# Kernel tuning notes

Measured on AMD Instinct MI355X. Metric: run time of the kernel, lower is better.

## Reference

```python
import jax, jax.numpy as jnp
import numpy as np

B, S, H, NH, I = 8, 1024, 1024, 16, 4096
HD = H // NH
EPS = 1e-6
NEG = -1e9


def _glorot(key, shape):
    lim = np.sqrt(6.0 / (shape[0] + shape[1]))
    return jax.random.uniform(key, shape, jnp.float32, -lim, lim)


def setup_inputs() -> dict:
    key = jax.random.key(0)
    ks = jax.random.split(key, 8)
    return {
        "inputs": jax.random.normal(ks[0], (B, S, H), jnp.float32),
        "inputs_mask": jnp.zeros((B, S), jnp.float32),  # 1.0 marks padding
        "attn_qkvw": _glorot(ks[1], (H, 3 * H)),
        "attn_qkvb": jnp.zeros((3 * H,), jnp.float32),
        "attn_ow": _glorot(ks[2], (H, H)),
        "attn_ob": jnp.zeros((H,), jnp.float32),
        "attn_nw": jnp.ones((H,), jnp.float32),
        "attn_nb": jnp.zeros((H,), jnp.float32),
        "inter_w": _glorot(ks[3], (H, I)),
        "inter_b": jnp.zeros((I,), jnp.float32),
        "output_w": _glorot(ks[4], (I, H)),
        "output_b": jnp.zeros((H,), jnp.float32),
        "ffn_nw": jnp.ones((H,), jnp.float32),
        "ffn_nb": jnp.zeros((H,), jnp.float32),
    }


def _layer_norm(x, g, b):
    m = jnp.mean(x, axis=-1, keepdims=True)
    v = jnp.mean(jnp.square(x - m), axis=-1, keepdims=True)
    return (x - m) * jax.lax.rsqrt(v + EPS) * g + b


def reference(inputs, inputs_mask, attn_qkvw, attn_qkvb, attn_ow, attn_ob,
              attn_nw, attn_nb, inter_w, inter_b, output_w, output_b,
              ffn_nw, ffn_nb):
    # ---- self-attention block (pre-LN) ----
    res = inputs
    x = _layer_norm(inputs, attn_nw, attn_nb)
    qkv = x @ attn_qkvw + attn_qkvb                      # [B,S,3H]
    q, k, v = jnp.split(qkv, 3, axis=-1)
    q = q.reshape(B, S, NH, HD)
    k = k.reshape(B, S, NH, HD)
    v = v.reshape(B, S, NH, HD)
    scale = 1.0 / np.sqrt(HD)
    scores = jnp.einsum("bqhd,bkhd->bhqk", q, k) * scale
    scores = scores + inputs_mask[:, None, None, :] * NEG
    probs = jax.nn.softmax(scores, axis=-1)
    ctx = jnp.einsum("bhqk,bkhd->bqhd", probs, v).reshape(B, S, H)
    attn_out = ctx @ attn_ow + attn_ob
    x = res + attn_out
    # ---- FFN block (pre-LN, ReLU) ----
    res2 = x
    y = _layer_norm(x, ffn_nw, ffn_nb)
    h = jax.nn.relu(y @ inter_w + inter_b)
    return res2 + h @ output_w + output_b
```

## Files before the change

kernel.cpp:

```cpp
#include <hip/hip_runtime.h>
#include <cstdint>
#include <cstddef>

typedef _Float16 f16;
typedef _Float16 half8 __attribute__((ext_vector_type(8)));
typedef _Float16 half4v __attribute__((ext_vector_type(4)));
typedef float floatx4 __attribute__((ext_vector_type(4)));
typedef float floatx16 __attribute__((ext_vector_type(16)));

__device__ __forceinline__ floatx4 mfma16(half8 a, half8 b, floatx4 c) {
    return __builtin_amdgcn_mfma_f32_16x16x32_f16(a, b, c, 0, 0, 0);
}
__device__ __forceinline__ floatx16 mfma32(half8 a, half8 b, floatx16 c) {
    return __builtin_amdgcn_mfma_f32_32x32x16_f16(a, b, c, 0, 0, 0);
}

__device__ __forceinline__ void async16(const f16* g, f16* l) {
    __builtin_amdgcn_global_load_lds(
        (const __attribute__((address_space(1))) unsigned int*)(uintptr_t)g,
        (__attribute__((address_space(3))) unsigned int*)(uintptr_t)l,
        16, 0, 0);
}

__global__ __launch_bounds__(256)
void ln_f16_kernel(const float* __restrict__ x, const float* __restrict__ g,
                   const float* __restrict__ be, f16* __restrict__ y)
{
    int row = blockIdx.x, t = threadIdx.x;
    const float* xr = x + (size_t)row * 1024;
    float4 v = *(const float4*)(xr + t * 4);
    float s1 = v.x + v.y + v.z + v.w;
    float s2 = v.x * v.x + v.y * v.y + v.z * v.z + v.w * v.w;
    #pragma unroll
    for (int off = 32; off >= 1; off >>= 1) {
        s1 += __shfl_xor(s1, off);
        s2 += __shfl_xor(s2, off);
    }
    __shared__ float r1[4], r2[4];
    if ((t & 63) == 0) { r1[t >> 6] = s1; r2[t >> 6] = s2; }
    __syncthreads();
    s1 = r1[0] + r1[1] + r1[2] + r1[3];
    s2 = r2[0] + r2[1] + r2[2] + r2[3];
    float mean = s1 * 0.0009765625f;
    float var  = s2 * 0.0009765625f - mean * mean;
    float rs = rsqrtf(var + 1e-6f);
    float4 gv = *(const float4*)(g + t * 4);
    float4 bv = *(const float4*)(be + t * 4);
    half4v o;
    o[0] = (f16)((v.x - mean) * rs * gv.x + bv.x);
    o[1] = (f16)((v.y - mean) * rs * gv.y + bv.y);
    o[2] = (f16)((v.z - mean) * rs * gv.z + bv.z);
    o[3] = (f16)((v.w - mean) * rs * gv.w + bv.w);
    *(half4v*)(y + (size_t)row * 1024 + t * 4) = o;
}

__global__ __launch_bounds__(256)
void transpose_f16_kernel(const float* __restrict__ W, f16* __restrict__ WT,
                          int R, int C)
{
    __shared__ float tile[32][33];
    int tx = threadIdx.x & 31, ty0 = threadIdx.x >> 5;
    int r0 = blockIdx.y * 32, c0 = blockIdx.x * 32;
    #pragma unroll
    for (int i = 0; i < 4; ++i)
        tile[ty0 + i * 8][tx] = W[(size_t)(r0 + ty0 + i * 8) * C + c0 + tx];
    __syncthreads();
    #pragma unroll
    for (int i = 0; i < 4; ++i)
        WT[(size_t)(c0 + ty0 + i * 8) * R + r0 + tx] = (f16)tile[tx][ty0 + i * 8];
}

__global__ __launch_bounds__(256, 2)
void gemm_kernel(const f16* __restrict__ A, const f16* __restrict__ BT,
                 const float* __restrict__ bias, const float* __restrict__ res,
                 float* __restrict__ Cf32, int M, int N, int K)
{
    __shared__ __align__(16) f16 As[128 * 64];
    __shared__ __align__(16) f16 Bs[128 * 64];
    int m0 = blockIdx.x * 128, n0 = blockIdx.y * 128;
    int t = threadIdx.x, lane = t & 63, wave = t >> 6;
    int quad = lane >> 4, l16 = lane & 15;
    int wm = (wave & 1) * 64, wn = (wave >> 1) * 64;
    int sw = l16 & 7;
    floatx4 acc[4][4] = {};

    for (int k0 = 0; k0 < K; k0 += 64) {
        __syncthreads();
        #pragma unroll
        for (int c = 0; c < 4; ++c) {
            int s = c * 256 + t;
            int row = s >> 3, phys = s & 7;
            int lg = phys ^ (row & 7);
            async16(A  + (size_t)(m0 + row) * K + k0 + lg * 8,
                    As + (size_t)(c * 256 + (t & ~63)) * 8);
            async16(BT + (size_t)(n0 + row) * K + k0 + lg * 8,
                    Bs + (size_t)(c * 256 + (t & ~63)) * 8);
        }
        __syncthreads();
        #pragma unroll
        for (int ks = 0; ks < 2; ++ks) {
            int ca = (ks * 4 + quad) ^ sw;
            half8 a[4], b[4];
            #pragma unroll
            for (int i = 0; i < 4; ++i) {
                a[i] = *(const half8*)(As + (wm + i * 16 + l16) * 64 + ca * 8);
                b[i] = *(const half8*)(Bs + (wn + i * 16 + l16) * 64 + ca * 8);
            }
            #pragma unroll
            for (int i = 0; i < 4; ++i)
                #pragma unroll
                for (int j = 0; j < 4; ++j)
                    acc[i][j] = mfma16(a[i], b[j], acc[i][j]);
        }
    }

    #pragma unroll
    for (int j = 0; j < 4; ++j) {
        int col = n0 + wn + j * 16 + l16;
        float bv = bias[col];
        #pragma unroll
        for (int i = 0; i < 4; ++i) {
            int rowb = m0 + wm + i * 16 + quad * 4;
            #pragma unroll
            for (int r = 0; r < 4; ++r) {
                float v = acc[i][j][r] + bv;
                size_t idx = (size_t)(rowb + r) * N + col;
                Cf32[idx] = v + res[idx];
            }
        }
    }
}

template<int MODE>
__global__ __launch_bounds__(256, 2)
void gemm_big_kernel(const f16* __restrict__ A, const f16* __restrict__ BT,
                     const float* __restrict__ bias, f16* __restrict__ Cf16,
                     f16* __restrict__ qb, f16* __restrict__ kb, f16* __restrict__ vb,
                     int M, int N, int K)
{
    __shared__ __align__(16) f16 As[256 * 64];
    __shared__ __align__(16) f16 Bs[128 * 64];
    int m0 = blockIdx.x * 256, n0 = blockIdx.y * 128;
    int t = threadIdx.x, lane = t & 63, wave = t >> 6;
    int l32 = lane & 31, kg = lane >> 5;
    int swz = l32 & 7;
    floatx16 acc[2][4];
    #pragma unroll
    for (int mi = 0; mi < 2; ++mi)
        #pragma unroll
        for (int jn = 0; jn < 4; ++jn)
            #pragma unroll
            for (int r = 0; r < 16; ++r) acc[mi][jn][r] = 0.f;

    for (int k0 = 0; k0 < K; k0 += 64) {
        __syncthreads();
        #pragma unroll
        for (int c = 0; c < 8; ++c) {
            int s = c * 256 + t;
            int row = s >> 3, phys = s & 7;
            int lg = phys ^ (row & 7);
            async16(A + (size_t)(m0 + row) * K + k0 + lg * 8,
                    As + (size_t)(c * 256 + (t & ~63)) * 8);
        }
        #pragma unroll
        for (int c = 0; c < 4; ++c) {
            int s = c * 256 + t;
            int row = s >> 3, phys = s & 7;
            int lg = phys ^ (row & 7);
            async16(BT + (size_t)(n0 + row) * K + k0 + lg * 8,
                    Bs + (size_t)(c * 256 + (t & ~63)) * 8);
        }
        __syncthreads();
        #pragma unroll
        for (int ss = 0; ss < 4; ++ss) {
            int ca = (ss * 2 + kg) ^ swz;
            half8 a[2], b[4];
            #pragma unroll
            for (int mi = 0; mi < 2; ++mi)
                a[mi] = *(const half8*)(As + (wave * 64 + mi * 32 + l32) * 64 + ca * 8);
            #pragma unroll
            for (int jn = 0; jn < 4; ++jn)
                b[jn] = *(const half8*)(Bs + (jn * 32 + l32) * 64 + ca * 8);
            #pragma unroll
            for (int mi = 0; mi < 2; ++mi)
                #pragma unroll
                for (int jn = 0; jn < 4; ++jn)
                    acc[mi][jn] = mfma32(a[mi], b[jn], acc[mi][jn]);
        }
    }

    #pragma unroll
    for (int mi = 0; mi < 2; ++mi) {
        int mbase = m0 + wave * 64 + mi * 32 + 4 * kg;
        #pragma unroll
        for (int jn = 0; jn < 4; ++jn) {
            int col = n0 + jn * 32 + l32;
            float bv = bias[col];
            if (MODE == 1) {
                #pragma unroll
                for (int reg = 0; reg < 16; ++reg) {
                    int row = mbase + (reg & 3) + 8 * (reg >> 2);
                    Cf16[(size_t)row * N + col] = (f16)fmaxf(acc[mi][jn][reg] + bv, 0.f);
                }
            } else {
                int part = col >> 10;
                int h = (col >> 6) & 15;
                int d = col & 63;
                if (part == 2) {
                    #pragma unroll
                    for (int rb = 0; rb < 4; ++rb) {
                        int m = mbase + 8 * rb;
                        int bb = m >> 10, s = m & 1023;
                        size_t bh = (size_t)bb * 16 + h;
                        half4v pv;
                        #pragma unroll
                        for (int r = 0; r < 4; ++r) pv[r] = (f16)(acc[mi][jn][rb * 4 + r] + bv);
                        *(half4v*)(vb + (bh * 64 + d) * 1024 + s) = pv;
                    }
                } else {
                    f16* dst0 = part == 0 ? qb : kb;
                    #pragma unroll
                    for (int reg = 0; reg < 16; ++reg) {
                        int m = mbase + (reg & 3) + 8 * (reg >> 2);
                        int bb = m >> 10, s = m & 1023;
                        size_t bh = (size_t)bb * 16 + h;
                        dst0[(bh * 1024 + s) * 64 + d] = (f16)(acc[mi][jn][reg] + bv);
                    }
                }
            }
        }
    }
}

__global__ __launch_bounds__(256)
void attn_kernel(const f16* __restrict__ qb, const f16* __restrict__ kb,
                 const f16* __restrict__ vb, const float* __restrict__ mask,
                 f16* __restrict__ ctx)
{
    const int S = 1024;
    int qt = blockIdx.x, h = blockIdx.y, b = blockIdx.z;
    size_t bh = (size_t)b * 16 + h;
    int t = threadIdx.x, lane = t & 63, wv = t >> 6;
    int quad = lane >> 4, l16 = lane & 15;
    int sw = l16 & 7;

    __shared__ __align__(16) f16 Ks[64 * 64];
    __shared__ __align__(16) f16 Vs[64 * 64];
    __shared__ __align__(16) f16 Ps[4][16 * 40];

    int q0 = qt * 64 + wv * 16;
    const f16* qrow = qb + (bh * 1024 + q0 + l16) * 64;
    half8 aq0 = *(const half8*)(qrow + quad * 8);
    half8 aq1 = *(const half8*)(qrow + 32 + quad * 8);

    floatx4 o[4] = {};
    float lsum[4] = {0.f, 0.f, 0.f, 0.f};
    const float scale = 0.125f;
    const float* mrow = mask + b * S;

    for (int kc = 0; kc < S; kc += 64) {
        __syncthreads();
        #pragma unroll
        for (int c = 0; c < 2; ++c) {
            int s = c * 256 + t;
            int row = s >> 3, phys = s & 7;
            int lg = phys ^ (row & 7);
            f16* lk = Ks + (size_t)(c * 256 + (t & ~63)) * 8;
            f16* lv = Vs + (size_t)(c * 256 + (t & ~63)) * 8;
            async16(kb + (bh * 1024 + kc + row) * 64 + lg * 8, lk);
            async16(vb + (bh * 64 + row) * 1024 + kc + lg * 8, lv);
        }
        __syncthreads();

        floatx4 sf[4];
        #pragma unroll
        for (int cg = 0; cg < 4; ++cg) {
            const f16* kr = Ks + (cg * 16 + l16) * 64;
            int c0 = quad ^ sw;
            half8 b0 = *(const half8*)(kr + c0 * 8);
            half8 b1 = *(const half8*)(kr + (c0 ^ 4) * 8);
            floatx4 z = {};
            sf[cg] = mfma16(aq1, b1, mfma16(aq0, b0, z));
        }
        #pragma unroll
        for (int cg = 0; cg < 4; ++cg) {
            float mk = mrow[kc + cg * 16 + l16] * (-1e9f);
            #pragma unroll
            for (int r = 0; r < 4; ++r) {
                float e = __expf(sf[cg][r] * scale + mk);
                lsum[r] += e;
                Ps[wv][(quad * 4 + r) * 40 + cg * 16 + l16] = (f16)e;
            }
        }
        half8 ap0 = *(const half8*)(Ps[wv] + l16 * 40 + quad * 8);
        half8 ap1 = *(const half8*)(Ps[wv] + l16 * 40 + 32 + quad * 8);
        #pragma unroll
        for (int td = 0; td < 4; ++td) {
            const f16* vr = Vs + (td * 16 + l16) * 64;
            int c0 = quad ^ sw;
            half8 bv0 = *(const half8*)(vr + c0 * 8);
            half8 bv1 = *(const half8*)(vr + (c0 ^ 4) * 8);
            o[td] = mfma16(ap0, bv0, o[td]);
            o[td] = mfma16(ap1, bv1, o[td]);
        }
    }

    #pragma unroll
    for (int r = 0; r < 4; ++r) {
        float s = lsum[r];
        s += __shfl_xor(s, 1); s += __shfl_xor(s, 2);
        s += __shfl_xor(s, 4); s += __shfl_xor(s, 8);
        lsum[r] = 1.f / s;
    }
    #pragma unroll
    for (int td = 0; td < 4; ++td)
        #pragma unroll
        for (int r = 0; r < 4; ++r)
            ctx[((size_t)b * 1024 + q0 + quad * 4 + r) * 1024 + h * 64 + td * 16 + l16]
                = (f16)(o[td][r] * lsum[r]);
}

extern "C" void kernel_launch(void* const* d_in, const int* in_sizes, int n_in,
                              void* d_out, int out_size, void* d_ws, size_t ws_size,
                              hipStream_t stream)
{
    const float* inputs = (const float*)d_in[0];
    const float* mask   = (const float*)d_in[1];
    const float* qkvw   = (const float*)d_in[2];
    const float* qkvb   = (const float*)d_in[3];
    const float* ow     = (const float*)d_in[4];
    const float* ob     = (const float*)d_in[5];
    const float* anw    = (const float*)d_in[6];
    const float* anb    = (const float*)d_in[7];
    const float* iw     = (const float*)d_in[8];
    const float* ib     = (const float*)d_in[9];
    const float* outw   = (const float*)d_in[10];
    const float* outb   = (const float*)d_in[11];
    const float* fnw    = (const float*)d_in[12];
    const float* fnb    = (const float*)d_in[13];
    float* out = (float*)d_out;

    const int M = 8192;
    uint8_t* ws = (uint8_t*)d_ws;
    f16* wT_qkv = (f16*)(ws + 0);
    f16* wT_o   = (f16*)(ws + 6291456);
    f16* wT_i   = (f16*)(ws + 8388608);
    f16* wT_out = (f16*)(ws + 16777216);
    f16* xln    = (f16*)(ws + 25165824);
    float* x1   = (float*)(ws + 41943040);
    f16* qbuf   = (f16*)(ws + 75497472);
    f16* kbuf   = (f16*)(ws + 92274688);
    f16* vbuf   = (f16*)(ws + 109051904);
    f16* ctx    = (f16*)(ws + 125829120);
    f16* hbuf   = (f16*)(ws + 75497472);

    transpose_f16_kernel<<<dim3(96, 32),  256, 0, stream>>>(qkvw, wT_qkv, 1024, 3072);
    transpose_f16_kernel<<<dim3(32, 32),  256, 0, stream>>>(ow,   wT_o,   1024, 1024);
    transpose_f16_kernel<<<dim3(128, 32), 256, 0, stream>>>(iw,   wT_i,   1024, 4096);
    transpose_f16_kernel<<<dim3(32, 128), 256, 0, stream>>>(outw, wT_out, 4096, 1024);

    ln_f16_kernel<<<8192, 256, 0, stream>>>(inputs, anw, anb, xln);

    gemm_big_kernel<2><<<dim3(32, 24), 256, 0, stream>>>(xln, wT_qkv, qkvb,
        nullptr, qbuf, kbuf, vbuf, M, 3072, 1024);

    attn_kernel<<<dim3(16, 16, 8), 256, 0, stream>>>(qbuf, kbuf, vbuf, mask, ctx);

    gemm_kernel<<<dim3(64, 8), 256, 0, stream>>>(ctx, wT_o, ob, inputs,
        x1, M, 1024, 1024);

    ln_f16_kernel<<<8192, 256, 0, stream>>>(x1, fnw, fnb, xln);

    gemm_big_kernel<1><<<dim3(32, 32), 256, 0, stream>>>(xln, wT_i, ib,
        hbuf, nullptr, nullptr, nullptr, M, 4096, 1024);

    gemm_kernel<<<dim3(64, 8), 256, 0, stream>>>(hbuf, wT_out, outb, x1,
        out, M, 1024, 4096);
}
```

Baseline: 482.1 us.

## Register-prefetch GEMM tiles, store residual in fp16, merge weight transposes

Both GEMM kernels drop the async global-to-LDS loads in favour of register prefetch of the next K tile, overlapping global loads with MFMA work. The small GEMM also moves to a K tile of 128 with a 16-way XOR swizzle, which doubles its LDS footprint. The intermediate residual x1 is stored in fp16 instead of fp32, halving its traffic, and a new LN kernel reads fp16 input. The four weight transposes are merged into one launch. The fp16 residual loses precision, and the extra registers and LDS may lower occupancy.

```diff
diff --git a/kernel.cpp b/kernel.cpp
--- a/kernel.cpp
+++ b/kernel.cpp
@@ -55,12 +55,42 @@
 }
 
 __global__ __launch_bounds__(256)
-void transpose_f16_kernel(const float* __restrict__ W, f16* __restrict__ WT,
-                          int R, int C)
+void ln_f16in_kernel(const f16* __restrict__ x, const float* __restrict__ g,
+                     const float* __restrict__ be, f16* __restrict__ y)
+{
+    int row = blockIdx.x, t = threadIdx.x;
+    half4v h = *(const half4v*)(x + (size_t)row * 1024 + t * 4);
+    float vx = (float)h[0], vy = (float)h[1], vz = (float)h[2], vw = (float)h[3];
+    float s1 = vx + vy + vz + vw;
+    float s2 = vx * vx + vy * vy + vz * vz + vw * vw;
+    #pragma unroll
+    for (int off = 32; off >= 1; off >>= 1) {
+        s1 += __shfl_xor(s1, off);
+        s2 += __shfl_xor(s2, off);
+    }
+    __shared__ float r1[4], r2[4];
+    if ((t & 63) == 0) { r1[t >> 6] = s1; r2[t >> 6] = s2; }
+    __syncthreads();
+    s1 = r1[0] + r1[1] + r1[2] + r1[3];
+    s2 = r2[0] + r2[1] + r2[2] + r2[3];
+    float mean = s1 * 0.0009765625f;
+    float var  = s2 * 0.0009765625f - mean * mean;
+    float rs = rsqrtf(var + 1e-6f);
+    float4 gv = *(const float4*)(g + t * 4);
+    float4 bv = *(const float4*)(be + t * 4);
+    half4v o;
+    o[0] = (f16)((vx - mean) * rs * gv.x + bv.x);
+    o[1] = (f16)((vy - mean) * rs * gv.y + bv.y);
+    o[2] = (f16)((vz - mean) * rs * gv.z + bv.z);
+    o[3] = (f16)((vw - mean) * rs * gv.w + bv.w);
+    *(half4v*)(y + (size_t)row * 1024 + t * 4) = o;
+}
+
+__device__ __forceinline__ void tr_tile(const float* W, f16* WT, int R, int C,
+                                        int bx, int by, int tx, int ty0)
 {
     __shared__ float tile[32][33];
-    int tx = threadIdx.x & 31, ty0 = threadIdx.x >> 5;
-    int r0 = blockIdx.y * 32, c0 = blockIdx.x * 32;
+    int r0 = by * 32, c0 = bx * 32;
     #pragma unroll
     for (int i = 0; i < 4; ++i)
         tile[ty0 + i * 8][tx] = W[(size_t)(r0 + ty0 + i * 8) * C + c0 + tx];
@@ -70,41 +100,65 @@
         WT[(size_t)(c0 + ty0 + i * 8) * R + r0 + tx] = (f16)tile[tx][ty0 + i * 8];
 }
 
+__global__ __launch_bounds__(256)
+void transpose_all_kernel(const float* __restrict__ qkvw, const float* __restrict__ ow,
+                          const float* __restrict__ iw, const float* __restrict__ outw,
+                          f16* __restrict__ wT_qkv, f16* __restrict__ wT_o,
+                          f16* __restrict__ wT_i, f16* __restrict__ wT_out)
+{
+    int id = blockIdx.x;
+    int tx = threadIdx.x & 31, ty0 = threadIdx.x >> 5;
+    if (id < 3072)       tr_tile(qkvw, wT_qkv, 1024, 3072, id % 96,  id / 96,  tx, ty0);
+    else if (id < 4096)  { id -= 3072; tr_tile(ow,   wT_o,   1024, 1024, id % 32,  id / 32,  tx, ty0); }
+    else if (id < 8192)  { id -= 4096; tr_tile(iw,   wT_i,   1024, 4096, id % 128, id / 128, tx, ty0); }
+    else                 { id -= 8192; tr_tile(outw, wT_out, 4096, 1024, id % 32,  id / 32,  tx, ty0); }
+}
+
+template<int OUT_F16>
 __global__ __launch_bounds__(256, 2)
 void gemm_kernel(const f16* __restrict__ A, const f16* __restrict__ BT,
-                 const float* __restrict__ bias, const float* __restrict__ res,
-                 float* __restrict__ Cf32, int M, int N, int K)
-{
-    __shared__ __align__(16) f16 As[128 * 64];
-    __shared__ __align__(16) f16 Bs[128 * 64];
+                 const float* __restrict__ bias, const void* __restrict__ resv,
+                 void* __restrict__ Cv, int M, int N, int K)
+{
+    __shared__ __align__(16) f16 As[128 * 128];
+    __shared__ __align__(16) f16 Bs[128 * 128];
     int m0 = blockIdx.x * 128, n0 = blockIdx.y * 128;
     int t = threadIdx.x, lane = t & 63, wave = t >> 6;
     int quad = lane >> 4, l16 = lane & 15;
     int wm = (wave & 1) * 64, wn = (wave >> 1) * 64;
-    int sw = l16 & 7;
     floatx4 acc[4][4] = {};
 
-    for (int k0 = 0; k0 < K; k0 += 64) {
-        __syncthreads();
-        #pragma unroll
-        for (int c = 0; c < 4; ++c) {
-            int s = c * 256 + t;
-            int row = s >> 3, phys = s & 7;
-            int lg = phys ^ (row & 7);
-            async16(A  + (size_t)(m0 + row) * K + k0 + lg * 8,
-                    As + (size_t)(c * 256 + (t & ~63)) * 8);
-            async16(BT + (size_t)(n0 + row) * K + k0 + lg * 8,
-                    Bs + (size_t)(c * 256 + (t & ~63)) * 8);
-        }
-        __syncthreads();
-        #pragma unroll
-        for (int ks = 0; ks < 2; ++ks) {
-            int ca = (ks * 4 + quad) ^ sw;
+    int rA = t >> 4;
+    int lg = (t & 15) ^ rA;
+    uint4 ra[8], rb[8];
+    #pragma unroll
+    for (int c = 0; c < 8; ++c) {
+        ra[c] = *(const uint4*)(A  + (size_t)(m0 + c * 16 + rA) * K + lg * 8);
+        rb[c] = *(const uint4*)(BT + (size_t)(n0 + c * 16 + rA) * K + lg * 8);
+    }
+
+    for (int k0 = 0; k0 < K; k0 += 128) {
+        __syncthreads();
+        #pragma unroll
+        for (int c = 0; c < 8; ++c) {
+            *(uint4*)(As + (c * 256 + t) * 8) = ra[c];
+            *(uint4*)(Bs + (c * 256 + t) * 8) = rb[c];
+        }
+        __syncthreads();
+        int kn = (k0 + 128 < K) ? k0 + 128 : k0;
+        #pragma unroll
+        for (int c = 0; c < 8; ++c) {
+            ra[c] = *(const uint4*)(A  + (size_t)(m0 + c * 16 + rA) * K + kn + lg * 8);
+            rb[c] = *(const uint4*)(BT + (size_t)(n0 + c * 16 + rA) * K + kn + lg * 8);
+        }
+        #pragma unroll
+        for (int ks = 0; ks < 4; ++ks) {
+            int ca = (ks * 4 + quad) ^ l16;
             half8 a[4], b[4];
             #pragma unroll
             for (int i = 0; i < 4; ++i) {
-                a[i] = *(const half8*)(As + (wm + i * 16 + l16) * 64 + ca * 8);
-                b[i] = *(const half8*)(Bs + (wn + i * 16 + l16) * 64 + ca * 8);
+                a[i] = *(const half8*)(As + (wm + i * 16 + l16) * 128 + ca * 8);
+                b[i] = *(const half8*)(Bs + (wn + i * 16 + l16) * 128 + ca * 8);
             }
             #pragma unroll
             for (int i = 0; i < 4; ++i)
@@ -123,9 +177,10 @@
             int rowb = m0 + wm + i * 16 + quad * 4;
             #pragma unroll
             for (int r = 0; r < 4; ++r) {
+                size_t idx = (size_t)(rowb + r) * N + col;
                 float v = acc[i][j][r] + bv;
-                size_t idx = (size_t)(rowb + r) * N + col;
-                Cf32[idx] = v + res[idx];
+                if (OUT_F16) ((f16*)Cv)[idx]   = (f16)(v + ((const float*)resv)[idx]);
+                else         ((float*)Cv)[idx] = v + (float)((const f16*)resv)[idx];
             }
         }
     }
@@ -152,25 +207,32 @@
             #pragma unroll
             for (int r = 0; r < 16; ++r) acc[mi][jn][r] = 0.f;
 
+    int rA = t >> 3;
+    int lg = (t & 7) ^ (rA & 7);
+    uint4 ra[8], rb[4];
+    #pragma unroll
+    for (int c = 0; c < 8; ++c)
+        ra[c] = *(const uint4*)(A + (size_t)(m0 + c * 32 + rA) * K + lg * 8);
+    #pragma unroll
+    for (int c = 0; c < 4; ++c)
+        rb[c] = *(const uint4*)(BT + (size_t)(n0 + c * 32 + rA) * K + lg * 8);
+
     for (int k0 = 0; k0 < K; k0 += 64) {
         __syncthreads();
         #pragma unroll
-        for (int c = 0; c < 8; ++c) {
-            int s = c * 256 + t;
-            int row = s >> 3, phys = s & 7;
-            int lg = phys ^ (row & 7);
-            async16(A + (size_t)(m0 + row) * K + k0 + lg * 8,
-                    As + (size_t)(c * 256 + (t & ~63)) * 8);
-        }
-        #pragma unroll
-        for (int c = 0; c < 4; ++c) {
-            int s = c * 256 + t;
-            int row = s >> 3, phys = s & 7;
-            int lg = phys ^ (row & 7);
-            async16(BT + (size_t)(n0 + row) * K + k0 + lg * 8,
-                    Bs + (size_t)(c * 256 + (t & ~63)) * 8);
-        }
-        __syncthreads();
+        for (int c = 0; c < 8; ++c)
+            *(uint4*)(As + (c * 256 + t) * 8) = ra[c];
+        #pragma unroll
+        for (int c = 0; c < 4; ++c)
+            *(uint4*)(Bs + (c * 256 + t) * 8) = rb[c];
+        __syncthreads();
+        int kn = (k0 + 64 < K) ? k0 + 64 : k0;
+        #pragma unroll
+        for (int c = 0; c < 8; ++c)
+            ra[c] = *(const uint4*)(A + (size_t)(m0 + c * 32 + rA) * K + kn + lg * 8);
+        #pragma unroll
+        for (int c = 0; c < 4; ++c)
+            rb[c] = *(const uint4*)(BT + (size_t)(n0 + c * 32 + rA) * K + kn + lg * 8);
         #pragma unroll
         for (int ss = 0; ss < 4; ++ss) {
             int ca = (ss * 2 + kg) ^ swz;
@@ -208,13 +270,13 @@
                 int d = col & 63;
                 if (part == 2) {
                     #pragma unroll
-                    for (int rb = 0; rb < 4; ++rb) {
-                        int m = mbase + 8 * rb;
+                    for (int rb2 = 0; rb2 < 4; ++rb2) {
+                        int m = mbase + 8 * rb2;
                         int bb = m >> 10, s = m & 1023;
                         size_t bh = (size_t)bb * 16 + h;
                         half4v pv;
                         #pragma unroll
-                        for (int r = 0; r < 4; ++r) pv[r] = (f16)(acc[mi][jn][rb * 4 + r] + bv);
+                        for (int r = 0; r < 4; ++r) pv[r] = (f16)(acc[mi][jn][rb2 * 4 + r] + bv);
                         *(half4v*)(vb + (bh * 64 + d) * 1024 + s) = pv;
                     }
                 } else {
@@ -347,17 +409,15 @@
     f16* wT_i   = (f16*)(ws + 8388608);
     f16* wT_out = (f16*)(ws + 16777216);
     f16* xln    = (f16*)(ws + 25165824);
-    float* x1   = (float*)(ws + 41943040);
+    f16* x1     = (f16*)(ws + 41943040);
     f16* qbuf   = (f16*)(ws + 75497472);
     f16* kbuf   = (f16*)(ws + 92274688);
     f16* vbuf   = (f16*)(ws + 109051904);
     f16* ctx    = (f16*)(ws + 125829120);
     f16* hbuf   = (f16*)(ws + 75497472);
 
-    transpose_f16_kernel<<<dim3(96, 32),  256, 0, stream>>>(qkvw, wT_qkv, 1024, 3072);
-    transpose_f16_kernel<<<dim3(32, 32),  256, 0, stream>>>(ow,   wT_o,   1024, 1024);
-    transpose_f16_kernel<<<dim3(128, 32), 256, 0, stream>>>(iw,   wT_i,   1024, 4096);
-    transpose_f16_kernel<<<dim3(32, 128), 256, 0, stream>>>(outw, wT_out, 4096, 1024);
+    transpose_all_kernel<<<12288, 256, 0, stream>>>(qkvw, ow, iw, outw,
+        wT_qkv, wT_o, wT_i, wT_out);
 
     ln_f16_kernel<<<8192, 256, 0, stream>>>(inputs, anw, anb, xln);
 
@@ -366,14 +426,14 @@
 
     attn_kernel<<<dim3(16, 16, 8), 256, 0, stream>>>(qbuf, kbuf, vbuf, mask, ctx);
 
-    gemm_kernel<<<dim3(64, 8), 256, 0, stream>>>(ctx, wT_o, ob, inputs,
-        x1, M, 1024, 1024);
-
-    ln_f16_kernel<<<8192, 256, 0, stream>>>(x1, fnw, fnb, xln);
+    gemm_kernel<1><<<dim3(64, 8), 256, 0, stream>>>(ctx, wT_o, ob,
+        inputs, x1, M, 1024, 1024);
+
+    ln_f16in_kernel<<<8192, 256, 0, stream>>>(x1, fnw, fnb, xln);
 
     gemm_big_kernel<1><<<dim3(32, 32), 256, 0, stream>>>(xln, wT_i, ib,
         hbuf, nullptr, nullptr, nullptr, M, 4096, 1024);
 
-    gemm_kernel<<<dim3(64, 8), 256, 0, stream>>>(hbuf, wT_out, outb, x1,
-        out, M, 1024, 4096);
-}
+    gemm_kernel<0><<<dim3(64, 8), 256, 0, stream>>>(hbuf, wT_out, outb,
+        x1, out, M, 1024, 4096);
+}
```

After: 1.053 ms. +118.3%, slower.
